# Kernel tuning notes

Measured on AMD Instinct MI355X. Metric: run time of the kernel, lower is better.

## Reference

```python
import jax, jax.numpy as jnp
from jax import lax
import numpy as np

B, C, T, V = 32, 256, 64, 48
NH = 4        # GroupAttn heads
G8 = 8        # num_heads // 4 gconv heads / tconv groups
C4 = C // 4
LN_EPS = 1e-5


def _ln(x, g, b):
    m = jnp.mean(x, axis=-1, keepdims=True)
    v = jnp.var(x, axis=-1, keepdims=True)
    return (x - m) * lax.rsqrt(v + LN_EPS) * g + b


def _conv2d(x, w, b, pad_t, groups):
    # x: (B, Cin, T, V), w: (Cout, Cin/groups, K, 1)
    y = lax.conv_general_dilated(x, w, (1, 1), (pad_t, (0, 0)),
                                 dimension_numbers=('NCHW', 'OIHW', 'NCHW'),
                                 feature_group_count=groups)
    return y + b[None, :, None, None]


def _group_attn(x, qkv_w, qkv_b, pw, pb):
    # x: (B, c, T, V) with c = C4; windows of Vg = V//3 joints
    Bc, c, Tc, Vc = x.shape
    G, Vg, hd = 3, Vc // 3, c // NH
    xp = x.reshape(Bc, c, Tc, G, Vg).transpose(0, 2, 3, 4, 1)       # (B,T,G,Vg,c)
    qkv = (xp @ qkv_w + qkv_b).reshape(Bc, Tc, G, Vg, 3, NH, hd)
    q, k, v = qkv[..., 0, :, :], qkv[..., 1, :, :], qkv[..., 2, :, :]
    # note: original scales by num_heads**-0.5 (not head_dim)
    attn = jnp.einsum('btgund,btgwnd->btgnuw', q, k) * (NH ** -0.5)
    attn = jax.nn.softmax(attn, axis=-1)
    out = jnp.einsum('btgnuw,btgwnd->btgund', attn, v).reshape(Bc, Tc, Vc, c)
    out = out @ pw + pb                                             # (B,T,V,3c)
    return out.transpose(0, 3, 1, 2)                                # (B,3c,T,V)


def setup_inputs() -> dict:
    key = jax.random.key(0)
    ks = jax.random.split(key, 16)
    w = lambda k, s: jax.random.normal(k, s, jnp.float32) * 0.02
    z = lambda n: jnp.zeros((n,), jnp.float32)
    return {
        'input': jax.random.normal(ks[0], (B, C, T, V), jnp.float32),
        'norm1_g': jnp.ones((C,), jnp.float32), 'norm1_b': z(C),
        'map_w': w(ks[1], (C, C)), 'map_b': z(C),
        'gconv': w(ks[2], (G8, V, V)),
        'tconv_w': w(ks[3], (C4, C4 // G8, 7, 1)), 'tconv_b': z(C4),
        'qkv_w0': w(ks[4], (C4, 3 * C4)), 'qkv_b0': z(3 * C4),
        'aproj_w0': w(ks[5], (C4, 3 * C4)), 'aproj_b0': z(3 * C4),
        'tcl_w0': w(ks[6], (C4, 3 * C4, 5, 1)), 'tcl_b0': z(C4),
        'qkv_w1': w(ks[7], (C4, 3 * C4)), 'qkv_b1': z(3 * C4),
        'aproj_w1': w(ks[8], (C4, 3 * C4)), 'aproj_b1': z(3 * C4),
        'tcl_w1': w(ks[9], (C4, 3 * C4, 5, 1)), 'tcl_b1': z(C4),
        'proj_w': w(ks[10], (C, C)), 'proj_b': z(C),
        'norm2_g': jnp.ones((C,), jnp.float32), 'norm2_b': z(C),
        'mlp_w1': w(ks[11], (C, 4 * C)), 'mlp_b1': z(4 * C),
        'mlp_w2': w(ks[12], (4 * C, C)), 'mlp_b2': z(C),
    }


def reference(input, norm1_g, norm1_b, map_w, map_b, gconv, tconv_w, tconv_b,
              qkv_w0, qkv_b0, aproj_w0, aproj_b0, tcl_w0, tcl_b0,
              qkv_w1, qkv_b1, aproj_w1, aproj_b1, tcl_w1, tcl_b1,
              proj_w, proj_b, norm2_g, norm2_b,
              mlp_w1, mlp_b1, mlp_w2, mlp_b2):
    x = input.transpose(0, 2, 3, 1)                                  # (B,T,V,C)
    skip = x
    f = (_ln(x, norm1_g, norm1_b) @ map_w + map_b).transpose(0, 3, 1, 2)  # (B,C,T,V)
    f_g, f_t = f[:, :C4], f[:, C4:2 * C4]
    f_a0, f_a1 = f[:, 2 * C4:3 * C4], f[:, 3 * C4:]
    # learned graph conv over joints, 8 channel groups
    cg = C4 // G8
    y0 = jnp.einsum('bgctu,gvu->bgctv', f_g.reshape(B, G8, cg, T, V), gconv)
    y0 = y0.reshape(B, C4, T, V)
    # grouped temporal conv, kernel 7, same padding
    y1 = _conv2d(f_t, tconv_w, tconv_b, (3, 3), G8)
    # windowed attention branches -> causal temporal conv (kernel 5)
    a0 = _group_attn(f_a0, qkv_w0, qkv_b0, aproj_w0, aproj_b0)
    y2 = _conv2d(a0, tcl_w0, tcl_b0, (4, 0), 1)
    a1 = _group_attn(f_a1, qkv_w1, qkv_b1, aproj_w1, aproj_b1)
    y3 = _conv2d(a1, tcl_w1, tcl_b1, (4, 0), 1)
    y = jnp.concatenate([y0, y1, y2, y3], axis=1).transpose(0, 2, 3, 1)  # (B,T,V,C)
    out = skip + (y @ proj_w + proj_b)
    h = jax.nn.gelu(_ln(out, norm2_g, norm2_b) @ mlp_w1 + mlp_b1, approximate=False)
    out = out + (h @ mlp_w2 + mlp_b2)
    return out.transpose(0, 3, 1, 2)                                 # (B,C,T,V)
```

## Files before the change

### kernel.cpp

```cpp
#include <hip/hip_runtime.h>
#include <hip/hip_bf16.h>
#include <math.h>

#define NB 32
#define CC 256
#define TT 64
#define VV 48
#define NTOK (NB*TT*VV)
#define LNE 1e-5f
#define PROWS 3264
#define A0P_USH ((size_t)NB*PROWS*192)

typedef __attribute__((ext_vector_type(8))) __bf16 bf16x8;
typedef __attribute__((ext_vector_type(4))) float f32x4;
typedef __attribute__((ext_vector_type(2))) long long2v;

__device__ inline float bfbits2f(unsigned int bits){
    union{unsigned int u; float f;} c; c.u = bits<<16; return c.f;
}
__device__ inline unsigned short f2bf(float x){
    union{ __bf16 h; unsigned short u; } c; c.h = (__bf16)x; return c.u;
}
__device__ inline unsigned char f2fp8(float x){
    int p = __builtin_amdgcn_cvt_pk_fp8_f32(x, x, 0, false);
    return (unsigned char)(p & 0xff);
}
__device__ inline unsigned int pk4fp8(float a, float b, float c, float d){
    int w = 0;
    w = __builtin_amdgcn_cvt_pk_fp8_f32(a, b, w, false);
    w = __builtin_amdgcn_cvt_pk_fp8_f32(c, d, w, true);
    return (unsigned int)w;
}
__device__ __forceinline__ void unpk8(uint4 u, float* d){
    d[0]=bfbits2f(u.x&0xffffu); d[1]=bfbits2f(u.x>>16);
    d[2]=bfbits2f(u.y&0xffffu); d[3]=bfbits2f(u.y>>16);
    d[4]=bfbits2f(u.z&0xffffu); d[5]=bfbits2f(u.z>>16);
    d[6]=bfbits2f(u.w&0xffffu); d[7]=bfbits2f(u.w>>16);
}
__device__ __forceinline__ float gelu4_fast(float x){
    float e = __expf(-1.702f * x);
    return (4.f * x) * __builtin_amdgcn_rcpf(1.f + e);
}

__device__ __forceinline__ void gll16(const char* g, char* l){
    __builtin_amdgcn_global_load_lds(
        (const __attribute__((address_space(1))) unsigned int*)g,
        (__attribute__((address_space(3))) unsigned int*)l, 16, 0, 0);
}

__global__ void prep_weights(const float* gconv, const float* tcl0, const float* tcl1,
                             const float* map_w, const float* proj_w,
                             const float* mlp_w1, const float* mlp_w2,
                             const float* qkv_w0, const float* qkv_w1,
                             const float* aproj_w0, const float* aproj_w1,
                             float* gct,
                             unsigned short* mapT, unsigned short* projT,
                             unsigned char* w1T8, unsigned char* w2T8,
                             unsigned short* tclT0, unsigned short* tclT1,
                             unsigned short* qkvT, unsigned short* aprojT){
    int tid = blockIdx.x*blockDim.x + threadIdx.x;
    int stride = gridDim.x*blockDim.x;
    for (int i = tid; i < 8*48*48; i += stride){
        int g = i/(48*48); int r = i%(48*48); int u = r/48; int v = r%48;
        gct[i] = gconv[(g*48+v)*48+u];
    }
    for (int i = tid; i < 64*960; i += stride){
        int o = i/960, col = i%960, kh = col/192, c = col%192;
        tclT0[i] = f2bf(tcl0[(o*192+c)*5+kh]);
        tclT1[i] = f2bf(tcl1[(o*192+c)*5+kh]);
    }
    for (int i = tid; i < 65536; i += stride){
        int n = i>>8, k = i&255;
        mapT[i] = f2bf(map_w[k*256+n]);
        projT[i] = f2bf(proj_w[k*256+n]);
    }
    for (int i = tid; i < 262144; i += stride){
        int n = i>>8, k = i&255;
        w1T8[i] = f2fp8(mlp_w1[k*1024+n] * 64.f);
    }
    for (int i = tid; i < 262144; i += stride){
        int n = i>>10, k = i&1023;
        w2T8[i] = f2fp8(mlp_w2[k*256+n] * 32.f);
    }
    for (int i = tid; i < 12288; i += stride){
        int n = i/64, k = i%64;
        qkvT[i]          = f2bf(qkv_w0[k*192+n]);
        qkvT[12288+i]    = f2bf(qkv_w1[k*192+n]);
        aprojT[i]        = f2bf(aproj_w0[k*192+n]);
        aprojT[12288+i]  = f2bf(aproj_w1[k*192+n]);
    }
}

__global__ __launch_bounds__(256) void xpose_ln1(const float* __restrict__ x,
        const float* __restrict__ g, const float* __restrict__ bb,
        unsigned short* __restrict__ A1, unsigned short* __restrict__ xskip){
    int bt = blockIdx.x; int b = bt/TT, t = bt%TT;
    __shared__ float X[48*257];
    __shared__ float S[4][48], SS[4][48], sm[48], sv[48];
    int tid = threadIdx.x;
    const float* xb = x + (size_t)b*256*3072 + (size_t)t*48;
    for (int it = 0; it < 12; it++){
        int idx = it*256 + tid;
        int c = idx/12, q = idx%12;
        float4 v = *(const float4*)(xb + (size_t)c*3072 + q*4);
        X[(q*4+0)*257 + c] = v.x;
        X[(q*4+1)*257 + c] = v.y;
        X[(q*4+2)*257 + c] = v.z;
        X[(q*4+3)*257 + c] = v.w;
    }
    __syncthreads();
    if (tid < 192){
        int v = tid % 48, w = tid / 48;
        float s = 0.f, ss = 0.f;
        for (int c = w*64; c < w*64+64; c++){
            float val = X[v*257 + c];
            s += val; ss += val*val;
        }
        S[w][v] = s; SS[w][v] = ss;
    }
    __syncthreads();
    if (tid < 48){
        float s = S[0][tid]+S[1][tid]+S[2][tid]+S[3][tid];
        float q = SS[0][tid]+SS[1][tid]+SS[2][tid]+SS[3][tid];
        float m = s*(1.f/256);
        sm[tid] = m; sv[tid] = rsqrtf(q*(1.f/256) - m*m + LNE);
    }
    __syncthreads();
    int nb = bt*48;
    for (int it = 0; it < 12; it++){
        int idx = it*256 + tid;
        int v = idx>>6, cq = idx&63;
        float m = sm[v], rs = sv[v];
        float4 g4 = *(const float4*)(g + cq*4);
        float4 b4 = *(const float4*)(bb + cq*4);
        float x0 = X[v*257 + cq*4+0], x1 = X[v*257 + cq*4+1];
        float x2 = X[v*257 + cq*4+2], x3 = X[v*257 + cq*4+3];
        ushort4 u;
        u.x = f2bf((x0-m)*rs*g4.x + b4.x);
        u.y = f2bf((x1-m)*rs*g4.y + b4.y);
        u.z = f2bf((x2-m)*rs*g4.z + b4.z);
        u.w = f2bf((x3-m)*rs*g4.w + b4.w);
        *(ushort4*)(A1 + (size_t)(nb+v)*256 + cq*4) = u;
        ushort4 s;
        s.x = f2bf(x0); s.y = f2bf(x1); s.z = f2bf(x2); s.w = f2bf(x3);
        *(ushort4*)(xskip + (size_t)(nb+v)*256 + cq*4) = s;
    }
}

__device__ __forceinline__ void stage_swz(const char* src, size_t rowbytes, char* lds,
                                          int nchunks, int tid){
    for (int c = tid; c < nchunks; c += 256){
        int p = c << 4;
        int r = p >> 7;
        int kl = (p & 127) ^ ((r & 7) << 4);
        gll16(src + (size_t)r*rowbytes + kl, lds + p);
    }
}

__device__ __forceinline__ bf16x8 frag_ld(const char* lds, int R, int kb){
    return *(const bf16x8*)(lds + R*128 + (kb ^ ((R & 7) << 4)));
}
__device__ __forceinline__ long2v frag_ld16(const char* lds, int R, int kb){
    return *(const long2v*)(lds + R*128 + (kb ^ ((R & 7) << 4)));
}

template<int KTOT, int EPI>
__global__ __launch_bounds__(512, 4) void mfma_gemm(
    const unsigned short* __restrict__ A, const unsigned short* __restrict__ BT,
    const float* __restrict__ bias,
    unsigned short* __restrict__ outH, unsigned char* __restrict__ outH8,
    int ncols, int nx){

    constexpr int BM = 192, BN = 128;
    constexpr int HALF = (BM+BN)*128;
    __shared__ __align__(16) char smem[2*HALF];
    int tid = threadIdx.x, lane = tid & 63;
    int wid = tid >> 6;
    int wm = wid >> 1, wn = wid & 1;
    int l15 = lane & 15, lq = lane >> 4;
    int bid = blockIdx.x;
    int per = gridDim.x >> 3;
    int wkid = (bid & 7)*per + (bid >> 3);
    int m0 = (wkid / nx) * BM, n0 = (wkid % nx) * BN;
    const size_t arb = KTOT*2, brb = KTOT*2;
    constexpr int KT = KTOT/64;

    const char* gA[3]; int loA[3];
    const char* gB[2]; int loB[2];
    {
        const char* Ab = (const char*)A + (size_t)m0*arb;
        const char* Bb = (const char*)BT + (size_t)n0*brb;
        #pragma unroll
        for (int i = 0; i < 3; i++){
            int c = tid + i*512;
            int p = c << 4, r = p >> 7;
            int kl = (p & 127) ^ ((r & 7) << 4);
            gA[i] = Ab + (size_t)r*arb + kl; loA[i] = p;
        }
        #pragma unroll
        for (int i = 0; i < 2; i++){
            int c = tid + i*512;
            int p = c << 4, r = p >> 7;
            int kl = (p & 127) ^ ((r & 7) << 4);
            gB[i] = Bb + (size_t)r*brb + kl; loB[i] = BM*128 + p;
        }
    }

    f32x4 acc[3][4];
    #pragma unroll
    for (int i = 0; i < 3; i++)
        #pragma unroll
        for (int j = 0; j < 4; j++){ f32x4 z = {0.f,0.f,0.f,0.f}; acc[i][j] = z; }

    #pragma unroll
    for (int i = 0; i < 3; i++) gll16(gA[i], smem + loA[i]);
    #pragma unroll
    for (int i = 0; i < 2; i++) gll16(gB[i], smem + loB[i]);

    int koff = 128;
    for (int kt = 0; kt < KT; kt++){
        char* cur = smem + (kt & 1)*HALF;
        if (kt + 1 < KT){
            char* nxt = smem + ((kt + 1) & 1)*HALF;
            #pragma unroll
            for (int i = 0; i < 3; i++) gll16(gA[i] + koff, nxt + loA[i]);
            #pragma unroll
            for (int i = 0; i < 2; i++) gll16(gB[i] + koff, nxt + loB[i]);
            koff += 128;
            asm volatile("s_waitcnt vmcnt(5)" ::: "memory");
        } else {
            asm volatile("s_waitcnt vmcnt(0)" ::: "memory");
        }
        __builtin_amdgcn_s_barrier();
        __builtin_amdgcn_sched_barrier(0);
        char* ldsA = cur;
        char* ldsB = cur + BM*128;
        #pragma unroll
        for (int ks = 0; ks < 2; ks++){
            bf16x8 a[3], b[4];
            int kb = ks*64 + lq*16;
            #pragma unroll
            for (int mf = 0; mf < 3; mf++) a[mf] = frag_ld(ldsA, wm*48 + mf*16 + l15, kb);
            #pragma unroll
            for (int nf = 0; nf < 4; nf++) b[nf] = frag_ld(ldsB, wn*64 + nf*16 + l15, kb);
            #pragma unroll
            for (int mf = 0; mf < 3; mf++)
                #pragma unroll
                for (int nf = 0; nf < 4; nf++)
                    acc[mf][nf] = __builtin_amdgcn_mfma_f32_16x16x32_bf16(a[mf], b[nf], acc[mf][nf], 0, 0, 0);
        }
        __builtin_amdgcn_sched_barrier(0);
        __builtin_amdgcn_s_barrier();
    }

    if constexpr (EPI == 4){
        unsigned short* Hs = (unsigned short*)smem;
        #pragma unroll
        for (int nf = 0; nf < 4; nf++){
            int col = wn*64 + nf*16 + l15;
            float bb = bias[n0 + col];
            #pragma unroll
            for (int mf = 0; mf < 3; mf++){
                int row = wm*48 + mf*16 + lq*4;
                f32x4 v = acc[mf][nf];
                #pragma unroll
                for (int r = 0; r < 4; r++)
                    Hs[(row+r)*136 + col] = f2bf(v[r] + bb);
            }
        }
        __syncthreads();
        for (int idx = tid; idx < 192*16; idx += 512){
            int row = idx >> 4, c8 = idx & 15;
            *(uint4*)(outH + (size_t)(m0+row)*ncols + n0 + c8*8) =
                *(const uint4*)(Hs + row*136 + c8*8);
        }
    }
}

__global__ __launch_bounds__(512, 4) void mfma_mlp1_fp8(
    const unsigned char* __restrict__ A, const unsigned char* __restrict__ BT,
    const float* __restrict__ bias, unsigned char* __restrict__ outH8){

    constexpr int BM = 192, BN = 128, NX = 8;
    constexpr int HALF = (BM+BN)*128;
    __shared__ __align__(16) char smem[2*HALF];
    int tid = threadIdx.x, lane = tid & 63;
    int wid = tid >> 6;
    int wm = wid >> 1, wn = wid & 1;
    int l15 = lane & 15, lq = lane >> 4;
    int bid = blockIdx.x;
    int per = gridDim.x >> 3;
    int wkid = (bid & 7)*per + (bid >> 3);
    int m0 = (wkid / NX) * BM, n0 = (wkid % NX) * BN;
    const size_t arb = 256, brb = 256;
    constexpr int KT = 2;

    const char* gA[3]; int loA[3];
    const char* gB[2]; int loB[2];
    {
        const char* Ab = (const char*)A + (size_t)m0*arb;
        const char* Bb = (const char*)BT + (size_t)n0*brb;
        #pragma unroll
        for (int i = 0; i < 3; i++){
            int c = tid + i*512;
            int p = c << 4, r = p >> 7;
            int kl = (p & 127) ^ ((r & 7) << 4);
            gA[i] = Ab + (size_t)r*arb + kl; loA[i] = p;
        }
        #pragma unroll
        for (int i = 0; i < 2; i++){
            int c = tid + i*512;
            int p = c << 4, r = p >> 7;
            int kl = (p & 127) ^ ((r & 7) << 4);
            gB[i] = Bb + (size_t)r*brb + kl; loB[i] = BM*128 + p;
        }
    }

    f32x4 acc[3][4];
    #pragma unroll
    for (int i = 0; i < 3; i++)
        #pragma unroll
        for (int j = 0; j < 4; j++){ f32x4 z = {0.f,0.f,0.f,0.f}; acc[i][j] = z; }

    #pragma unroll
    for (int i = 0; i < 3; i++) gll16(gA[i], smem + loA[i]);
    #pragma unroll
    for (int i = 0; i < 2; i++) gll16(gB[i], smem + loB[i]);

    int koff = 128;
    for (int kt = 0; kt < KT; kt++){
        char* cur = smem + (kt & 1)*HALF;
        if (kt + 1 < KT){
            char* nxt = smem + ((kt + 1) & 1)*HALF;
            #pragma unroll
            for (int i = 0; i < 3; i++) gll16(gA[i] + koff, nxt + loA[i]);
            #pragma unroll
            for (int i = 0; i < 2; i++) gll16(gB[i] + koff, nxt + loB[i]);
            koff += 128;
            asm volatile("s_waitcnt vmcnt(5)" ::: "memory");
        } else {
            asm volatile("s_waitcnt vmcnt(0)" ::: "memory");
        }
        __builtin_amdgcn_s_barrier();
        __builtin_amdgcn_sched_barrier(0);
        char* ldsA = cur;
        char* ldsB = cur + BM*128;
        #pragma unroll
        for (int hf = 0; hf < 2; hf++){
            long2v a[3], b[4];
            int kb = hf*64 + lq*16;
            #pragma unroll
            for (int mf = 0; mf < 3; mf++) a[mf] = frag_ld16(ldsA, wm*48 + mf*16 + l15, kb);
            #pragma unroll
            for (int nf = 0; nf < 4; nf++) b[nf] = frag_ld16(ldsB, wn*64 + nf*16 + l15, kb);
            #pragma unroll
            for (int mf = 0; mf < 3; mf++)
                #pragma unroll
                for (int nf = 0; nf < 4; nf++){
                    acc[mf][nf] = __builtin_amdgcn_mfma_f32_16x16x32_fp8_fp8(a[mf][0], b[nf][0], acc[mf][nf], 0, 0, 0);
                    acc[mf][nf] = __builtin_amdgcn_mfma_f32_16x16x32_fp8_fp8(a[mf][1], b[nf][1], acc[mf][nf], 0, 0, 0);
                }
        }
        __builtin_amdgcn_sched_barrier(0);
        __builtin_amdgcn_s_barrier();
    }

    unsigned char* Hc = (unsigned char*)smem;
    #pragma unroll
    for (int nf = 0; nf < 4; nf++){
        int col = wn*64 + nf*16 + l15;
        float bb = bias[n0 + col];
        #pragma unroll
        for (int mf = 0; mf < 3; mf++){
            int row = wm*48 + mf*16 + lq*4;
            f32x4 v = acc[mf][nf];
            #pragma unroll
            for (int r = 0; r < 4; r++){
                float t0 = gelu4_fast(v[r]*0.015625f + bb);
                Hc[(row+r)*144 + col] = f2fp8(t0);
            }
        }
    }
    __syncthreads();
    for (int idx = tid; idx < 192*8; idx += 512){
        int row = idx >> 3, c16 = idx & 7;
        *(uint4*)(outH8 + (size_t)(m0+row)*1024 + n0 + c16*16) =
            *(const uint4*)(Hc + row*144 + c16*16);
    }
}

__global__ __launch_bounds__(512, 4) void mfma_final_fp8(
    const unsigned char* __restrict__ A, const unsigned char* __restrict__ BT,
    const float* __restrict__ bias, const unsigned short* __restrict__ extraH,
    float* __restrict__ outF){

    constexpr int BM = 192, BN = 128, NX = 2;
    constexpr int HALF = (BM+BN)*128;
    __shared__ __align__(16) char smem[2*HALF];
    int tid = threadIdx.x, lane = tid & 63;
    int wid = tid >> 6;
    int wm = wid >> 1, wn = wid & 1;
    int l15 = lane & 15, lq = lane >> 4;
    int bid = blockIdx.x;
    int per = gridDim.x >> 3;
    int wkid = (bid & 7)*per + (bid >> 3);
    int m0 = (wkid / NX) * BM, n0 = (wkid % NX) * BN;
    const size_t arb = 1024, brb = 1024;
    constexpr int KT = 8;

    const char* gA[3]; int loA[3];
    const char* gB[2]; int loB[2];
    {
        const char* Ab = (const char*)A + (size_t)m0*arb;
        const char* Bb = (const char*)BT + (size_t)n0*brb;
        #pragma unroll
        for (int i = 0; i < 3; i++){
            int c = tid + i*512;
            int p = c << 4, r = p >> 7;
            int kl = (p & 127) ^ ((r & 7) << 4);
            gA[i] = Ab + (size_t)r*arb + kl; loA[i] = p;
        }
        #pragma unroll
        for (int i = 0; i < 2; i++){
            int c = tid + i*512;
            int p = c << 4, r = p >> 7;
            int kl = (p & 127) ^ ((r & 7) << 4);
            gB[i] = Bb + (size_t)r*brb + kl; loB[i] = BM*128 + p;
        }
    }

    f32x4 acc[3][4];
    #pragma unroll
    for (int i = 0; i < 3; i++)
        #pragma unroll
        for (int j = 0; j < 4; j++){ f32x4 z = {0.f,0.f,0.f,0.f}; acc[i][j] = z; }

    #pragma unroll
    for (int i = 0; i < 3; i++) gll16(gA[i], smem + loA[i]);
    #pragma unroll
    for (int i = 0; i < 2; i++) gll16(gB[i], smem + loB[i]);

    int koff = 128;
    for (int kt = 0; kt < KT; kt++){
        char* cur = smem + (kt & 1)*HALF;
        if (kt + 1 < KT){
            char* nxt = smem + ((kt + 1) & 1)*HALF;
            #pragma unroll
            for (int i = 0; i < 3; i++) gll16(gA[i] + koff, nxt + loA[i]);
            #pragma unroll
            for (int i = 0; i < 2; i++) gll16(gB[i] + koff, nxt + loB[i]);
            koff += 128;
            asm volatile("s_waitcnt vmcnt(5)" ::: "memory");
        } else {
            asm volatile("s_waitcnt vmcnt(0)" ::: "memory");
        }
        __builtin_amdgcn_s_barrier();
        __builtin_amdgcn_sched_barrier(0);
        char* ldsA = cur;
        char* ldsB = cur + BM*128;
        #pragma unroll
        for (int hf = 0; hf < 2; hf++){
            long2v a[3], b[4];
            int kb = hf*64 + lq*16;
            #pragma unroll
            for (int mf = 0; mf < 3; mf++) a[mf] = frag_ld16(ldsA, wm*48 + mf*16 + l15, kb);
            #pragma unroll
            for (int nf = 0; nf < 4; nf++) b[nf] = frag_ld16(ldsB, wn*64 + nf*16 + l15, kb);
            #pragma unroll
            for (int mf = 0; mf < 3; mf++)
                #pragma unroll
                for (int nf = 0; nf < 4; nf++){
                    acc[mf][nf] = __builtin_amdgcn_mfma_f32_16x16x32_fp8_fp8(a[mf][0], b[nf][0], acc[mf][nf], 0, 0, 0);
                    acc[mf][nf] = __builtin_amdgcn_mfma_f32_16x16x32_fp8_fp8(a[mf][1], b[nf][1], acc[mf][nf], 0, 0, 0);
                }
        }
        __builtin_amdgcn_sched_barrier(0);
        __builtin_amdgcn_s_barrier();
    }

    float* Tt = (float*)smem;
    #pragma unroll
    for (int p = 0; p < 2; p++){
        __syncthreads();
        #pragma unroll
        for (int q = 0; q < 2; q++){
            int nf = 2*p + q;
            int col = wn*64 + nf*16 + l15;
            int vc  = wn*32 + q*16 + l15;
            float bb = bias[n0 + col];
            #pragma unroll
            for (int mf = 0; mf < 3; mf++){
                int tl = wm*48 + mf*16 + lq*4;
                f32x4 v = acc[mf][nf];
                #pragma unroll
                for (int r = 0; r < 4; r++){
                    float resid = bfbits2f(extraH[(size_t)(m0+tl+r)*256 + n0 + col]);
                    Tt[vc*197 + tl + r] = v[r]*0.0078125f + bb + resid;
                }
            }
        }
        __syncthreads();
        {
            int lc = tid & 63, btl = (tid>>6)&3, dup = tid>>8;
            int ch = 32*p + lc + (lc & 32);
            int gtok = m0 + btl*48;
            int bg = gtok/3072, t = (gtok%3072)/48;
            float* dst = outF + ((size_t)(bg*256 + n0 + ch)*64 + t)*48 + dup*24;
            const float* tr = Tt + lc*197 + btl*48 + dup*24;
            #pragma unroll
            for (int j = 0; j < 6; j++)
                *(float4*)(dst + j*4) = *(const float4*)(tr + j*4);
        }
    }
}

__global__ __launch_bounds__(512, 2) void proj_ln2(
    const unsigned short* __restrict__ A, const unsigned short* __restrict__ BT,
    const float* __restrict__ bias, const unsigned short* __restrict__ xskip,
    const float* __restrict__ n2g, const float* __restrict__ n2b,
    unsigned short* __restrict__ outtH, unsigned char* __restrict__ xn8){

    constexpr int BM = 192, BN = 256, KTOT = 256;
    constexpr int HALF = (BM+BN)*128;
    __shared__ __align__(16) char smem[2*HALF];
    int tid = threadIdx.x, lane = tid & 63;
    int wid = tid >> 6;
    int wm = wid >> 1, wn = wid & 1;
    int l15 = lane & 15, lq = lane >> 4;
    int bid = blockIdx.x;
    int per = gridDim.x >> 3;
    int wkid = (bid & 7)*per + (bid >> 3);
    int m0 = wkid * BM;
    const size_t arb = KTOT*2, brb = KTOT*2;
    constexpr int KT = KTOT/64;

    const char* gA[3]; int loA[3];
    const char* gB[4]; int loB[4];
    {
        const char* Ab = (const char*)A + (size_t)m0*arb;
        const char* Bb = (const char*)BT;
        #pragma unroll
        for (int i = 0; i < 3; i++){
            int c = tid + i*512;
            int p = c << 4, r = p >> 7;
            int kl = (p & 127) ^ ((r & 7) << 4);
            gA[i] = Ab + (size_t)r*arb + kl; loA[i] = p;
        }
        #pragma unroll
        for (int i = 0; i < 4; i++){
            int c = tid + i*512;
            int p = c << 4, r = p >> 7;
            int kl = (p & 127) ^ ((r & 7) << 4);
            gB[i] = Bb + (size_t)r*brb + kl; loB[i] = BM*128 + p;
        }
    }

    f32x4 acc[3][8];
    #pragma unroll
    for (int i = 0; i < 3; i++)
        #pragma unroll
        for (int j = 0; j < 8; j++){ f32x4 z = {0.f,0.f,0.f,0.f}; acc[i][j] = z; }

    #pragma unroll
    for (int i = 0; i < 3; i++) gll16(gA[i], smem + loA[i]);
    #pragma unroll
    for (int i = 0; i < 4; i++) gll16(gB[i], smem + loB[i]);

    int koff = 128;
    for (int kt = 0; kt < KT; kt++){
        char* cur = smem + (kt & 1)*HALF;
        if (kt + 1 < KT){
            char* nxt = smem + ((kt + 1) & 1)*HALF;
            #pragma unroll
            for (int i = 0; i < 3; i++) gll16(gA[i] + koff, nxt + loA[i]);
            #pragma unroll
            for (int i = 0; i < 4; i++) gll16(gB[i] + koff, nxt + loB[i]);
            koff += 128;
            asm volatile("s_waitcnt vmcnt(7)" ::: "memory");
        } else {
            asm volatile("s_waitcnt vmcnt(0)" ::: "memory");
        }
        __builtin_amdgcn_s_barrier();
        __builtin_amdgcn_sched_barrier(0);
        char* ldsA = cur;
        char* ldsB = cur + BM*128;
        #pragma unroll
        for (int ks = 0; ks < 2; ks++){
            bf16x8 a[3], b[8];
            int kb = ks*64 + lq*16;
            #pragma unroll
            for (int mf = 0; mf < 3; mf++) a[mf] = frag_ld(ldsA, wm*48 + mf*16 + l15, kb);
            #pragma unroll
            for (int nf = 0; nf < 8; nf++) b[nf] = frag_ld(ldsB, wn*128 + nf*16 + l15, kb);
            #pragma unroll
            for (int mf = 0; mf < 3; mf++)
                #pragma unroll
                for (int nf = 0; nf < 8; nf++)
                    acc[mf][nf] = __builtin_amdgcn_mfma_f32_16x16x32_bf16(a[mf], b[nf], acc[mf][nf], 0, 0, 0);
        }
        __builtin_amdgcn_sched_barrier(0);
        __builtin_amdgcn_s_barrier();
    }

    unsigned short* Hs = (unsigned short*)smem;
    float* Sred = (float*)(smem + 101376);
    float s_acc[3][4], ss_acc[3][4];
    #pragma unroll
    for (int i = 0; i < 3; i++)
        #pragma unroll
        for (int r = 0; r < 4; r++){ s_acc[i][r] = 0.f; ss_acc[i][r] = 0.f; }

    #pragma unroll
    for (int nf = 0; nf < 8; nf++){
        int col = wn*128 + nf*16 + l15;
        float bb = bias[col];
        #pragma unroll
        for (int mf = 0; mf < 3; mf++){
            int row = wm*48 + mf*16 + lq*4;
            f32x4 v = acc[mf][nf];
            #pragma unroll
            for (int r = 0; r < 4; r++){
                float sk = bfbits2f(xskip[(size_t)(m0+row+r)*256 + col]);
                unsigned short us = f2bf(v[r] + bb + sk);
                Hs[(row+r)*264 + col] = us;
                float tf = bfbits2f(us);
                s_acc[mf][r] += tf; ss_acc[mf][r] += tf*tf;
            }
        }
    }
    #pragma unroll
    for (int mf = 0; mf < 3; mf++)
        #pragma unroll
        for (int r = 0; r < 4; r++){
            float s = s_acc[mf][r], ss = ss_acc[mf][r];
            #pragma unroll
            for (int d = 1; d < 16; d <<= 1){
                s  += __shfl_xor(s, d);
                ss += __shfl_xor(ss, d);
            }
            if (l15 == 0){
                int row = wm*48 + mf*16 + lq*4 + r;
                Sred[wn*192 + row] = s;
                Sred[384 + wn*192 + row] = ss;
            }
        }
    __syncthreads();
    if (tid < 192){
        float s  = Sred[tid] + Sred[192+tid];
        float ss = Sred[384+tid] + Sred[576+tid];
        float m = s*(1.f/256);
        Sred[tid] = m;
        Sred[192+tid] = rsqrtf(ss*(1.f/256) - m*m + LNE);
    }
    __syncthreads();
    for (int idx = tid; idx < 192*32; idx += 512){
        int row = idx >> 5, c8 = idx & 31;
        uint4 hv = *(const uint4*)(Hs + row*264 + c8*8);
        *(uint4*)(outtH + (size_t)(m0+row)*256 + c8*8) = hv;
        float v[8]; unpk8(hv, v);
        float m = Sred[row], rs = Sred[192+row];
        float xv[8];
        #pragma unroll
        for (int j = 0; j < 8; j++)
            xv[j] = (v[j]-m)*rs*n2g[c8*8 + j] + n2b[c8*8 + j];
        uint2 o;
        o.x = pk4fp8(xv[0], xv[1], xv[2], xv[3]);
        o.y = pk4fp8(xv[4], xv[5], xv[6], xv[7]);
        *(uint2*)(xn8 + (size_t)(m0+row)*256 + c8*8) = o;
    }
}

template<int EPI>
__global__ __launch_bounds__(256) void gemm_k64(
    const unsigned short* __restrict__ A, int arb,
    const unsigned short* __restrict__ BT,
    const float* __restrict__ bias,
    unsigned short* __restrict__ out){
    __shared__ __align__(16) char smem[96*128 + 192*128];
    char* ldsA = smem;
    char* ldsB = smem + 96*128;
    int tid = threadIdx.x, lane = tid & 63;
    int wid = tid >> 6, wm = wid >> 1, wn = wid & 1;
    int l15 = lane & 15, lq = lane >> 4;
    int m0 = blockIdx.x * 96;

    stage_swz((const char*)A + (size_t)m0*arb, arb, ldsA, 96*8, tid);
    stage_swz((const char*)BT, 128, ldsB, 192*8, tid);
    __syncthreads();

    f32x4 acc[3][6];
    #pragma unroll
    for (int i = 0; i < 3; i++)
        #pragma unroll
        for (int j = 0; j < 6; j++){ f32x4 z = {0.f,0.f,0.f,0.f}; acc[i][j] = z; }

    #pragma unroll
    for (int ks = 0; ks < 2; ks++){
        bf16x8 a[3], b[6];
        int kb = ks*64 + lq*16;
        #pragma unroll
        for (int mf = 0; mf < 3; mf++) a[mf] = frag_ld(ldsA, wm*48 + mf*16 + l15, kb);
        #pragma unroll
        for (int nf = 0; nf < 6; nf++) b[nf] = frag_ld(ldsB, wn*96 + nf*16 + l15, kb);
        #pragma unroll
        for (int mf = 0; mf < 3; mf++)
            #pragma unroll
            for (int nf = 0; nf < 6; nf++)
                acc[mf][nf] = __builtin_amdgcn_mfma_f32_16x16x32_bf16(a[mf], b[nf], acc[mf][nf], 0, 0, 0);
    }

    size_t row0;
    if constexpr (EPI == 0) row0 = (size_t)m0;
    else {
        int b = m0/3072;
        row0 = (size_t)b*PROWS + 192 + (m0 - b*3072);
    }
    #pragma unroll
    for (int nf = 0; nf < 6; nf++){
        int col = wn*96 + nf*16 + l15;
        float bb = bias[col];
        #pragma unroll
        for (int mf = 0; mf < 3; mf++){
            size_t rr = row0 + wm*48 + mf*16 + lq*4;
            f32x4 v = acc[mf][nf];
            #pragma unroll
            for (int r = 0; r < 4; r++)
                out[(rr+r)*192 + col] = f2bf(v[r] + bb);
        }
    }
}

__global__ __launch_bounds__(192) void attn_win(
        const unsigned short* __restrict__ qkvbuf,
        unsigned short* __restrict__ attnout){
    int win = blockIdx.x, br = blockIdx.y;
    size_t base = (size_t)br*NTOK + (size_t)win*48;
    __shared__ float Q[48*196];
    int tid = threadIdx.x;
    const unsigned short* src = qkvbuf + base*192;
    for (int i = 0; i < 6; i++){
        int ch = i*192 + tid;
        int v = ch/24, c8 = ch%24;
        uint4 u = *(const uint4*)(src + (size_t)v*192 + c8*8);
        unpk8(u, &Q[v*196 + c8*8]);
    }
    __syncthreads();
    int u = tid & 15, gh = tid >> 4, g = gh >> 2, h = gh & 3;
    int ru = g*16 + u;
    float qreg[16];
    #pragma unroll
    for (int d = 0; d < 16; d++) qreg[d] = Q[ru*196 + h*16 + d];
    float sc[16]; float mx = -1e30f;
    #pragma unroll
    for (int w = 0; w < 16; w++){
        float s = 0.f;
        #pragma unroll
        for (int d = 0; d < 16; d++) s += qreg[d]*Q[(g*16+w)*196 + 64 + h*16 + d];
        s *= 0.5f; sc[w] = s; mx = fmaxf(mx, s);
    }
    float sum = 0.f;
    #pragma unroll
    for (int w = 0; w < 16; w++){ sc[w] = __expf(sc[w]-mx); sum += sc[w]; }
    float inv = __builtin_amdgcn_rcpf(sum);
    unsigned int w32[8];
    #pragma unroll
    for (int dp = 0; dp < 8; dp++){
        float o0 = 0.f, o1 = 0.f;
        #pragma unroll
        for (int w = 0; w < 16; w++){
            float p = sc[w];
            o0 += p*Q[(g*16+w)*196 + 128 + h*16 + dp*2];
            o1 += p*Q[(g*16+w)*196 + 128 + h*16 + dp*2+1];
        }
        w32[dp] = (unsigned int)f2bf(o0*inv) | ((unsigned int)f2bf(o1*inv) << 16);
    }
    unsigned short* dst = attnout + (base + ru)*64 + h*16;
    uint4 q0; q0.x=w32[0]; q0.y=w32[1]; q0.z=w32[2]; q0.w=w32[3];
    uint4 q1; q1.x=w32[4]; q1.y=w32[5]; q1.z=w32[6]; q1.w=w32[7];
    *(uint4*)(dst)   = q0;
    *(uint4*)(dst+8) = q1;
}

__global__ __launch_bounds__(256) void tcl_mfma(const unsigned short* __restrict__ A0p,
        const unsigned short* __restrict__ BT, const float* __restrict__ tb,
        unsigned short* __restrict__ ybf, int outoff){
    constexpr int HALF = (192+64)*128;
    __shared__ __align__(16) char smem[2*HALF];
    int tid = threadIdx.x, lane = tid & 63;
    int wid = tid >> 6;
    int l15 = lane & 15, lq = lane >> 4;
    int bid = blockIdx.x;
    int per = gridDim.x >> 3;
    int wkid = (bid & 7)*per + (bid >> 3);
    int m0 = wkid * 192;
    int b = m0 / 3072;
    long brow0 = (long)b*PROWS + 192 + (m0 - b*3072);

    const char* gA[6]; int loA[6];
    const char* gB[2]; int loB[2];
    {
        const char* Ab = (const char*)A0p + (brow0 - 192)*384;
        #pragma unroll
        for (int i = 0; i < 6; i++){
            int c = tid + i*256;
            int p = c << 4, r = p >> 7;
            int kl = (p & 127) ^ ((r & 7) << 4);
            gA[i] = Ab + (size_t)r*384 + kl; loA[i] = p;
        }
        #pragma unroll
        for (int i = 0; i < 2; i++){
            int c = tid + i*256;
            int p = c << 4, r = p >> 7;
            int kl = (p & 127) ^ ((r & 7) << 4);
            gB[i] = (const char*)BT + (size_t)r*1920 + kl; loB[i] = 192*128 + p;
        }
    }

    f32x4 acc[3][4];
    #pragma unroll
    for (int i = 0; i < 3; i++)
        #pragma unroll
        for (int j = 0; j < 4; j++){ f32x4 z = {0.f,0.f,0.f,0.f}; acc[i][j] = z; }

    #pragma unroll
    for (int i = 0; i < 6; i++) gll16(gA[i], smem + loA[i]);
    #pragma unroll
    for (int i = 0; i < 2; i++) gll16(gB[i], smem + loB[i]);

    long offA = 0; int kc3 = 0; int offB = 0;
    for (int kt = 0; kt < 15; kt++){
        char* cur = smem + (kt & 1)*HALF;
        if (kt + 1 < 15){
            char* nxt = smem + ((kt + 1) & 1)*HALF;
            if (kc3 == 2){ offA += 18432 - 256; kc3 = 0; }
            else         { offA += 128; kc3++; }
            offB += 128;
            #pragma unroll
            for (int i = 0; i < 6; i++) gll16(gA[i] + offA, nxt + loA[i]);
            #pragma unroll
            for (int i = 0; i < 2; i++) gll16(gB[i] + offB, nxt + loB[i]);
            asm volatile("s_waitcnt vmcnt(8)" ::: "memory");
        } else {
            asm volatile("s_waitcnt vmcnt(0)" ::: "memory");
        }
        __builtin_amdgcn_s_barrier();
        __builtin_amdgcn_sched_barrier(0);
        char* ldsA = cur;
        char* ldsB = cur + 192*128;
        #pragma unroll
        for (int ks = 0; ks < 2; ks++){
            bf16x8 a[3], bb[4];
            int kb = ks*64 + lq*16;
            #pragma unroll
            for (int mf = 0; mf < 3; mf++) a[mf] = frag_ld(ldsA, wid*48 + mf*16 + l15, kb);
            #pragma unroll
            for (int nf = 0; nf < 4; nf++) bb[nf] = frag_ld(ldsB, nf*16 + l15, kb);
            #pragma unroll
            for (int mf = 0; mf < 3; mf++)
                #pragma unroll
                for (int nf = 0; nf < 4; nf++)
                    acc[mf][nf] = __builtin_amdgcn_mfma_f32_16x16x32_bf16(a[mf], bb[nf], acc[mf][nf], 0, 0, 0);
        }
        __builtin_amdgcn_sched_barrier(0);
        __builtin_amdgcn_s_barrier();
    }
    #pragma unroll
    for (int nf = 0; nf < 4; nf++){
        int col = nf*16 + l15;
        float bb = tb[col];
        #pragma unroll
        for (int mf = 0; mf < 3; mf++){
            int tok = m0 + wid*48 + mf*16 + lq*4;
            f32x4 v = acc[mf][nf];
            #pragma unroll
            for (int r = 0; r < 4; r++)
                ybf[(size_t)(tok+r)*256 + outoff + col] = f2bf(v[r] + bb);
        }
    }
}

__global__ __launch_bounds__(256) void y0_kernel(const unsigned short* __restrict__ fbf,
        const float* __restrict__ gct, unsigned short* __restrict__ ybf){
    int bt = blockIdx.x; int nb = bt*VV;
    __shared__ float X[48*68];
    for (int it = 0; it < 2; it++){
        int idx = it*256 + threadIdx.x;
        if (idx < 384){
            int v = idx >> 3, c8 = idx & 7;
            uint4 u = *(const uint4*)(fbf + (size_t)(nb+v)*256 + c8*8);
            unpk8(u, &X[v*68 + c8*8]);
        }
    }
    __syncthreads();
    int c = threadIdx.x % 64, vv = threadIdx.x / 64;
    int g = c >> 3;
    float acc[12] = {};
    for (int u = 0; u < 48; u++){
        float xv = X[u*68 + c];
        const float* gr = gct + (size_t)(g*48+u)*48 + vv*12;
        float4 g0 = *(const float4*)(gr);
        float4 g1 = *(const float4*)(gr+4);
        float4 g2 = *(const float4*)(gr+8);
        acc[0]+=xv*g0.x; acc[1]+=xv*g0.y; acc[2]+=xv*g0.z;  acc[3]+=xv*g0.w;
        acc[4]+=xv*g1.x; acc[5]+=xv*g1.y; acc[6]+=xv*g1.z;  acc[7]+=xv*g1.w;
        acc[8]+=xv*g2.x; acc[9]+=xv*g2.y; acc[10]+=xv*g2.z; acc[11]+=xv*g2.w;
    }
    #pragma unroll
    for (int j = 0; j < 12; j++)
        ybf[(size_t)(nb + vv*12 + j)*256 + c] = f2bf(acc[j]);
}

__global__ __launch_bounds__(256) void y1_kernel(const unsigned short* __restrict__ fbf,
        const float* __restrict__ tw, const float* __restrict__ tb, unsigned short* __restrict__ ybf){
    int bt = blockIdx.x; int b = bt/TT, t = bt%TT;
    __shared__ unsigned short W[7*48*64];
    int tid = threadIdx.x;
    for (int idx = tid; idx < 2688; idx += 256){
        int kh = idx/384, rem = idx - kh*384;
        int v = rem >> 3, c8 = rem & 7;
        int tt = t + kh - 3;
        uint4 u; u.x = 0; u.y = 0; u.z = 0; u.w = 0;
        if (tt >= 0 && tt < TT)
            u = *(const uint4*)(fbf + ((size_t)(b*TT+tt)*VV + v)*256 + 64 + c8*8);
        *(uint4*)(&W[idx*8]) = u;
    }
    __syncthreads();
    int o = tid & 63, vv = tid >> 6;
    int g = o >> 3;
    float bv = tb[o];
    float acc[12];
    #pragma unroll
    for (int j = 0; j < 12; j++) acc[j] = bv;
    for (int kh = 0; kh < 7; kh++){
        float wk[8];
        #pragma unroll
        for (int ci = 0; ci < 8; ci++) wk[ci] = tw[(o*8+ci)*7 + kh];
        const unsigned short* base = &W[kh*3072 + g*8];
        #pragma unroll
        for (int j = 0; j < 12; j++){
            uint4 u = *(const uint4*)(base + (vv*12 + j)*64);
            float fv[8]; unpk8(u, fv);
            acc[j] += fv[0]*wk[0]+fv[1]*wk[1]+fv[2]*wk[2]+fv[3]*wk[3]
                    + fv[4]*wk[4]+fv[5]*wk[5]+fv[6]*wk[6]+fv[7]*wk[7];
        }
    }
    int nb = bt*VV;
    #pragma unroll
    for (int j = 0; j < 12; j++)
        ybf[(size_t)(nb + vv*12 + j)*256 + 64 + o] = f2bf(acc[j]);
}

extern "C" void kernel_launch(void* const* d_in, const int* in_sizes, int n_in,
                              void* d_out, int out_size, void* d_ws, size_t ws_size,
                              hipStream_t stream){
    const float* input   = (const float*)d_in[0];
    const float* n1g     = (const float*)d_in[1];
    const float* n1b     = (const float*)d_in[2];
    const float* map_w   = (const float*)d_in[3];
    const float* map_b   = (const float*)d_in[4];
    const float* gconv   = (const float*)d_in[5];
    const float* tconv_w = (const float*)d_in[6];
    const float* tconv_b = (const float*)d_in[7];
    const float* qkv_w0  = (const float*)d_in[8];
    const float* qkv_b0  = (const float*)d_in[9];
    const float* aproj_w0= (const float*)d_in[10];
    const float* aproj_b0= (const float*)d_in[11];
    const float* tcl_w0  = (const float*)d_in[12];
    const float* tcl_b0  = (const float*)d_in[13];
    const float* qkv_w1  = (const float*)d_in[14];
    const float* qkv_b1  = (const float*)d_in[15];
    const float* aproj_w1= (const float*)d_in[16];
    const float* aproj_b1= (const float*)d_in[17];
    const float* tcl_w1  = (const float*)d_in[18];
    const float* tcl_b1  = (const float*)d_in[19];
    const float* proj_w  = (const float*)d_in[20];
    const float* proj_b  = (const float*)d_in[21];
    const float* n2g     = (const float*)d_in[22];
    const float* n2b     = (const float*)d_in[23];
    const float* mlp_w1  = (const float*)d_in[24];
    const float* mlp_b1  = (const float*)d_in[25];
    const float* mlp_w2  = (const float*)d_in[26];
    const float* mlp_b2  = (const float*)d_in[27];

    const size_t Nt = NTOK;
    if (ws_size < 354050048ull) return;

    char* base = (char*)d_ws;
    unsigned short* outtH  = (unsigned short*)base;
    unsigned short* fbf    = (unsigned short*)(base + 100663296);
    unsigned short* a0p    = (unsigned short*)(base + 150994944);
    unsigned short* qkvbuf = (unsigned short*)(base + 191102976);
    unsigned short* attnout= (unsigned short*)(base + 266600448);
    unsigned short* A1     = (unsigned short*)(base + 301989888);
    char* wp = base + 352321536;
    float* gct            = (float*)wp;
    unsigned short* mapT  = (unsigned short*)(wp + 73728);
    unsigned short* projT = mapT + 65536;
    unsigned short* w1T   = projT + 65536;
    unsigned char* w2T8   = (unsigned char*)(w1T + 262144);
    unsigned char* w1T8   = w2T8 + 262144;
    unsigned short* tclT0 = w1T + 262144 + 262144;
    unsigned short* tclT1 = tclT0 + 61440;
    unsigned short* qkvT  = tclT1 + 61440;
    unsigned short* aprojT= qkvT + 24576;

    unsigned char* h8   = (unsigned char*)fbf;
    unsigned char* xn8  = (unsigned char*)A1;
    unsigned short* ybf = (unsigned short*)d_out;
    unsigned short* xskip = ybf + (size_t)256*Nt;
    float* dout = (float*)d_out;

    prep_weights<<<256, 256, 0, stream>>>(gconv, tcl_w0, tcl_w1, map_w, proj_w, mlp_w1, mlp_w2,
                                          qkv_w0, qkv_w1, aproj_w0, aproj_w1,
                                          gct, mapT, projT, w1T8, w2T8, tclT0, tclT1, qkvT, aprojT);
    xpose_ln1<<<NB*TT, 256, 0, stream>>>(input, n1g, n1b, A1, xskip);
    mfma_gemm<256,4><<<1024, 512, 0, stream>>>(A1, mapT, map_b, fbf, nullptr, 256, 2);
    hipMemsetAsync(a0p, 0, A0P_USH*sizeof(unsigned short), stream);
    gemm_k64<0><<<1024, 256, 0, stream>>>(fbf + 128, 512, qkvT,         qkv_b0, qkvbuf);
    gemm_k64<0><<<1024, 256, 0, stream>>>(fbf + 192, 512, qkvT + 12288, qkv_b1, qkvbuf + (size_t)Nt*192);
    attn_win<<<dim3(2048,2), 192, 0, stream>>>(qkvbuf, attnout);
    y0_kernel<<<NB*TT, 256, 0, stream>>>(fbf, gct, ybf);
    y1_kernel<<<NB*TT, 256, 0, stream>>>(fbf, tconv_w, tconv_b, ybf);
    gemm_k64<1><<<1024, 256, 0, stream>>>(attnout,                 128, aprojT,         aproj_b0, a0p);
    tcl_mfma<<<NTOK/192, 256, 0, stream>>>(a0p, tclT0, tcl_b0, ybf, 128);
    gemm_k64<1><<<1024, 256, 0, stream>>>(attnout + (size_t)Nt*64, 128, aprojT + 12288, aproj_b1, a0p);
    tcl_mfma<<<NTOK/192, 256, 0, stream>>>(a0p, tclT1, tcl_b1, ybf, 192);
    proj_ln2<<<512, 512, 0, stream>>>(ybf, projT, proj_b, xskip, n2g, n2b, outtH, xn8);
    mfma_mlp1_fp8<<<4096, 512, 0, stream>>>(xn8, w1T8, mlp_b1, h8);
    mfma_final_fp8<<<1024, 512, 0, stream>>>(h8, w2T8, mlp_b2, outtH, dout);
}
```

Before: 509.0 us.

## Replace grouped temporal conv y1 with padded-buffer bf16 MFMA GEMM

The scalar grouped temporal convolution (kernel 7) is replaced by a new pad kernel that copies the y1 channel slice into a time-padded buffer, followed by an MFMA GEMM that treats the 7 taps as K-steps over a block-diagonal densified weight matrix. The goal is to move this branch onto matrix cores and reuse the double-buffered LDS GEMM pattern already used by tcl_mfma. In exchange it adds an extra pass over the activations, does 8x redundant MACs on the zero entries of the dense weights, and reuses the A1 and base workspace regions as scratch.

```diff
diff --git a/kernel.cpp b/kernel.cpp
--- a/kernel.cpp
+++ b/kernel.cpp
@@ -9,6 +9,7 @@
 #define NTOK (NB*TT*VV)
 #define LNE 1e-5f
 #define PROWS 3264
+#define PR7 3360
 #define A0P_USH ((size_t)NB*PROWS*192)
 
 typedef __attribute__((ext_vector_type(8))) __bf16 bf16x8;
@@ -53,11 +54,13 @@
                              const float* mlp_w1, const float* mlp_w2,
                              const float* qkv_w0, const float* qkv_w1,
                              const float* aproj_w0, const float* aproj_w1,
+                             const float* tconv,
                              float* gct,
                              unsigned short* mapT, unsigned short* projT,
                              unsigned char* w1T8, unsigned char* w2T8,
                              unsigned short* tclT0, unsigned short* tclT1,
-                             unsigned short* qkvT, unsigned short* aprojT){
+                             unsigned short* qkvT, unsigned short* aprojT,
+                             unsigned short* w1yT){
     int tid = blockIdx.x*blockDim.x + threadIdx.x;
     int stride = gridDim.x*blockDim.x;
     for (int i = tid; i < 8*48*48; i += stride){
@@ -88,6 +91,10 @@
         qkvT[12288+i]    = f2bf(qkv_w1[k*192+n]);
         aprojT[i]        = f2bf(aproj_w0[k*192+n]);
         aprojT[12288+i]  = f2bf(aproj_w1[k*192+n]);
+    }
+    for (int i = tid; i < 64*448; i += stride){
+        int o = i/448, k = i%448, kh = k>>6, ch = k&63;
+        w1yT[i] = (ch>>3 == o>>3) ? f2bf(tconv[(o*8 + (ch&7))*7 + kh]) : (unsigned short)0;
     }
 }
 
@@ -879,6 +886,114 @@
     }
 }
 
+__global__ __launch_bounds__(256) void pad_y1(const unsigned short* __restrict__ fbf,
+        unsigned short* __restrict__ pad){
+    int i = blockIdx.x*256 + threadIdx.x;
+    int c8 = i & 7; int pr = i >> 3;
+    int b = pr / PR7; int r = pr - b*PR7;
+    int tr = r - 144;
+    uint4 u; u.x = 0; u.y = 0; u.z = 0; u.w = 0;
+    if (tr >= 0 && tr < 3072)
+        u = *(const uint4*)(fbf + ((size_t)b*3072 + tr)*256 + 64 + c8*8);
+    *(uint4*)(pad + (size_t)pr*64 + c8*8) = u;
+}
+
+__global__ __launch_bounds__(256) void y1_mfma(const unsigned short* __restrict__ pad,
+        const unsigned short* __restrict__ BT, const float* __restrict__ tb,
+        unsigned short* __restrict__ ybf){
+    constexpr int HALF = (192+64)*128;
+    __shared__ __align__(16) char smem[2*HALF];
+    int tid = threadIdx.x, lane = tid & 63;
+    int wid = tid >> 6;
+    int l15 = lane & 15, lq = lane >> 4;
+    int bid = blockIdx.x;
+    int per = gridDim.x >> 3;
+    int wkid = (bid & 7)*per + (bid >> 3);
+    int m0 = wkid * 192;
+    int b = m0 / 3072;
+
+    const char* gA[6]; int loA[6];
+    const char* gB[2]; int loB[2];
+    {
+        const char* Ab = (const char*)pad + ((size_t)b*PR7 + (m0 - b*3072)) * 128;
+        #pragma unroll
+        for (int i = 0; i < 6; i++){
+            int c = tid + i*256;
+            int p = c << 4, r = p >> 7;
+            int kl = (p & 127) ^ ((r & 7) << 4);
+            gA[i] = Ab + (size_t)r*128 + kl; loA[i] = p;
+        }
+        #pragma unroll
+        for (int i = 0; i < 2; i++){
+            int c = tid + i*256;
+            int p = c << 4, r = p >> 7;
+            int kl = (p & 127) ^ ((r & 7) << 4);
+            gB[i] = (const char*)BT + (size_t)r*896 + kl; loB[i] = 192*128 + p;
+        }
+    }
+
+    f32x4 acc[3][4];
+    #pragma unroll
+    for (int i = 0; i < 3; i++)
+        #pragma unroll
+        for (int j = 0; j < 4; j++){ f32x4 z = {0.f,0.f,0.f,0.f}; acc[i][j] = z; }
+
+    #pragma unroll
+    for (int i = 0; i < 6; i++) gll16(gA[i], smem + loA[i]);
+    #pragma unroll
+    for (int i = 0; i < 2; i++) gll16(gB[i], smem + loB[i]);
+
+    int offA = 0, offB = 0;
+    for (int kt = 0; kt < 7; kt++){
+        char* cur = smem + (kt & 1)*HALF;
+        if (kt + 1 < 7){
+            char* nxt = smem + ((kt + 1) & 1)*HALF;
+            offA += 6144;
+            offB += 128;
+            #pragma unroll
+            for (int i = 0; i < 6; i++) gll16(gA[i] + offA, nxt + loA[i]);
+            #pragma unroll
+            for (int i = 0; i < 2; i++) gll16(gB[i] + offB, nxt + loB[i]);
+            asm volatile("s_waitcnt vmcnt(8)" ::: "memory");
+        } else {
+            asm volatile("s_waitcnt vmcnt(0)" ::: "memory");
+        }
+        __builtin_amdgcn_s_barrier();
+        __builtin_amdgcn_sched_barrier(0);
+        char* ldsA = cur;
+        char* ldsB = cur + 192*128;
+        #pragma unroll
+        for (int ks = 0; ks < 2; ks++){
+            bf16x8 a[3], bb[4];
+            int kb = ks*64 + lq*16;
+            #pragma unroll
+            for (int mf = 0; mf < 3; mf++) a[mf] = frag_ld(ldsA, wid*48 + mf*16 + l15, kb);
+            #pragma unroll
+            for (int nf = 0; nf < 4; nf++) bb[nf] = frag_ld(ldsB, nf*16 + l15, kb);
+            #pragma unroll
+            for (int mf = 0; mf < 3; mf++)
+                #pragma unroll
+                for (int nf = 0; nf < 4; nf++)
+                    acc[mf][nf] = __builtin_amdgcn_mfma_f32_16x16x32_bf16(a[mf], bb[nf], acc[mf][nf], 0, 0, 0);
+        }
+        __builtin_amdgcn_sched_barrier(0);
+        __builtin_amdgcn_s_barrier();
+    }
+    #pragma unroll
+    for (int nf = 0; nf < 4; nf++){
+        int col = nf*16 + l15;
+        float bb = tb[col];
+        #pragma unroll
+        for (int mf = 0; mf < 3; mf++){
+            int tok = m0 + wid*48 + mf*16 + lq*4;
+            f32x4 v = acc[mf][nf];
+            #pragma unroll
+            for (int r = 0; r < 4; r++)
+                ybf[(size_t)(tok+r)*256 + 64 + col] = f2bf(v[r] + bb);
+        }
+    }
+}
+
 __global__ __launch_bounds__(256) void y0_kernel(const unsigned short* __restrict__ fbf,
         const float* __restrict__ gct, unsigned short* __restrict__ ybf){
     int bt = blockIdx.x; int nb = bt*VV;
@@ -908,46 +1023,6 @@
     #pragma unroll
     for (int j = 0; j < 12; j++)
         ybf[(size_t)(nb + vv*12 + j)*256 + c] = f2bf(acc[j]);
-}
-
-__global__ __launch_bounds__(256) void y1_kernel(const unsigned short* __restrict__ fbf,
-        const float* __restrict__ tw, const float* __restrict__ tb, unsigned short* __restrict__ ybf){
-    int bt = blockIdx.x; int b = bt/TT, t = bt%TT;
-    __shared__ unsigned short W[7*48*64];
-    int tid = threadIdx.x;
-    for (int idx = tid; idx < 2688; idx += 256){
-        int kh = idx/384, rem = idx - kh*384;
-        int v = rem >> 3, c8 = rem & 7;
-        int tt = t + kh - 3;
-        uint4 u; u.x = 0; u.y = 0; u.z = 0; u.w = 0;
-        if (tt >= 0 && tt < TT)
-            u = *(const uint4*)(fbf + ((size_t)(b*TT+tt)*VV + v)*256 + 64 + c8*8);
-        *(uint4*)(&W[idx*8]) = u;
-    }
-    __syncthreads();
-    int o = tid & 63, vv = tid >> 6;
-    int g = o >> 3;
-    float bv = tb[o];
-    float acc[12];
-    #pragma unroll
-    for (int j = 0; j < 12; j++) acc[j] = bv;
-    for (int kh = 0; kh < 7; kh++){
-        float wk[8];
-        #pragma unroll
-        for (int ci = 0; ci < 8; ci++) wk[ci] = tw[(o*8+ci)*7 + kh];
-        const unsigned short* base = &W[kh*3072 + g*8];
-        #pragma unroll
-        for (int j = 0; j < 12; j++){
-            uint4 u = *(const uint4*)(base + (vv*12 + j)*64);
-            float fv[8]; unpk8(u, fv);
-            acc[j] += fv[0]*wk[0]+fv[1]*wk[1]+fv[2]*wk[2]+fv[3]*wk[3]
-                    + fv[4]*wk[4]+fv[5]*wk[5]+fv[6]*wk[6]+fv[7]*wk[7];
-        }
-    }
-    int nb = bt*VV;
-    #pragma unroll
-    for (int j = 0; j < 12; j++)
-        ybf[(size_t)(nb + vv*12 + j)*256 + 64 + o] = f2bf(acc[j]);
 }
 
 extern "C" void kernel_launch(void* const* d_in, const int* in_sizes, int n_in,
@@ -1006,13 +1081,15 @@
 
     unsigned char* h8   = (unsigned char*)fbf;
     unsigned char* xn8  = (unsigned char*)A1;
+    unsigned short* y1pad = A1;
+    unsigned short* w1yT  = (unsigned short*)base;
     unsigned short* ybf = (unsigned short*)d_out;
     unsigned short* xskip = ybf + (size_t)256*Nt;
     float* dout = (float*)d_out;
 
     prep_weights<<<256, 256, 0, stream>>>(gconv, tcl_w0, tcl_w1, map_w, proj_w, mlp_w1, mlp_w2,
-                                          qkv_w0, qkv_w1, aproj_w0, aproj_w1,
-                                          gct, mapT, projT, w1T8, w2T8, tclT0, tclT1, qkvT, aprojT);
+                                          qkv_w0, qkv_w1, aproj_w0, aproj_w1, tconv_w,
+                                          gct, mapT, projT, w1T8, w2T8, tclT0, tclT1, qkvT, aprojT, w1yT);
     xpose_ln1<<<NB*TT, 256, 0, stream>>>(input, n1g, n1b, A1, xskip);
     mfma_gemm<256,4><<<1024, 512, 0, stream>>>(A1, mapT, map_b, fbf, nullptr, 256, 2);
     hipMemsetAsync(a0p, 0, A0P_USH*sizeof(unsigned short), stream);
@@ -1020,7 +1097,8 @@
     gemm_k64<0><<<1024, 256, 0, stream>>>(fbf + 192, 512, qkvT + 12288, qkv_b1, qkvbuf + (size_t)Nt*192);
     attn_win<<<dim3(2048,2), 192, 0, stream>>>(qkvbuf, attnout);
     y0_kernel<<<NB*TT, 256, 0, stream>>>(fbf, gct, ybf);
-    y1_kernel<<<NB*TT, 256, 0, stream>>>(fbf, tconv_w, tconv_b, ybf);
+    pad_y1<<<(NB*PR7*8)/256, 256, 0, stream>>>(fbf, y1pad);
+    y1_mfma<<<NTOK/192, 256, 0, stream>>>(y1pad, w1yT, tconv_b, ybf);
     gemm_k64<1><<<1024, 256, 0, stream>>>(attnout,                 128, aprojT,         aproj_b0, a0p);
     tcl_mfma<<<NTOK/192, 256, 0, stream>>>(a0p, tclT0, tcl_b0, ybf, 128);
     gemm_k64<1><<<1024, 256, 0, stream>>>(attnout + (size_t)Nt*64, 128, aprojT + 12288, aproj_b1, a0p);
```

After: 458.5 us. -9.9%, faster.
